# Performance work log

Measured on AMD Instinct MI355X. Metric: run time of the kernel, lower is better.

The kernel has to match this reference:

```python
import jax, jax.numpy as jnp
import numpy as np

N_HEAD = 8
D_MODEL = 512
D_K = 64
D_V = 64


def setup_inputs() -> dict:
    key = jax.random.key(0)
    ks = jax.random.split(key, 12)
    B, L = 2, 2048
    q = jax.random.normal(ks[0], (B, L, D_MODEL), dtype=jnp.float32)
    k = jax.random.normal(ks[1], (B, L, D_MODEL), dtype=jnp.float32)
    v = jax.random.normal(ks[2], (B, L, D_MODEL), dtype=jnp.float32)
    mask = jnp.ones((B, L, L), dtype=jnp.int32)
    s = 1.0 / np.sqrt(D_MODEL)
    Wq = jax.random.uniform(ks[3], (D_MODEL, N_HEAD * D_K), jnp.float32, -s, s)
    bq = jax.random.uniform(ks[4], (N_HEAD * D_K,), jnp.float32, -s, s)
    Wk = jax.random.uniform(ks[5], (D_MODEL, N_HEAD * D_K), jnp.float32, -s, s)
    bk = jax.random.uniform(ks[6], (N_HEAD * D_K,), jnp.float32, -s, s)
    Wv = jax.random.uniform(ks[7], (D_MODEL, N_HEAD * D_V), jnp.float32, -s, s)
    bv = jax.random.uniform(ks[8], (N_HEAD * D_V,), jnp.float32, -s, s)
    so = 1.0 / np.sqrt(N_HEAD * D_V)
    Wo = jax.random.uniform(ks[9], (N_HEAD * D_V, D_MODEL), jnp.float32, -so, so)
    bo = jax.random.uniform(ks[10], (D_MODEL,), jnp.float32, -so, so)
    return {"q": q, "k": k, "v": v, "mask": mask,
            "Wq": Wq, "bq": bq, "Wk": Wk, "bk": bk,
            "Wv": Wv, "bv": bv, "Wo": Wo, "bo": bo}


def reference(q, k, v, mask, Wq, bq, Wk, bk, Wv, bv, Wo, bo):
    B, Lq, _ = q.shape
    Lk = k.shape[1]
    residual = q
    # project and split heads: [B, L, H, d] -> [H, B, L, d]
    qh = (q @ Wq + bq).reshape(B, Lq, N_HEAD, D_K).transpose(2, 0, 1, 3)
    kh = (k @ Wk + bk).reshape(B, Lk, N_HEAD, D_K).transpose(2, 0, 1, 3)
    vh = (v @ Wv + bv).reshape(B, Lk, N_HEAD, D_V).transpose(2, 0, 1, 3)
    # NOTE: original code uses temperature = d_k (not sqrt(d_k))
    attn = jnp.einsum('hbqd,hbkd->hbqk', qh / D_K, kh)
    attn = jnp.where(mask[None, :, :, :] == 0, -1e9, attn)
    attn = jax.nn.softmax(attn, axis=-1)  # dropout is identity at eval
    ctx = jnp.einsum('hbqk,hbkv->hbqv', attn, vh)  # [H, B, Lq, d_v]
    out = ctx.transpose(1, 2, 0, 3).reshape(B, Lq, N_HEAD * D_V)
    out = out @ Wo + bo + residual
    attn_out = attn.reshape(N_HEAD * B, Lq, Lk)  # matches original return layout
    return out, attn_out
```

## Files before the change

kernel.cpp:

```cpp
#include <hip/hip_runtime.h>
#include <hip/hip_bf16.h>
#include <cstdint>
#include <cstddef>

#define NH 8
#define DMODEL 512
#define DHEAD 64
#define BB 2
#define SEQ 2048

typedef __bf16 bf16x8 __attribute__((ext_vector_type(8)));
typedef float f32x4 __attribute__((ext_vector_type(4)));
typedef unsigned short u16;
typedef unsigned int u32;

__device__ __forceinline__ float bf2f(u16 u) {
  return __uint_as_float(((u32)u) << 16);
}
__device__ __forceinline__ u16 f2bf(float f) {
  u32 x = __float_as_uint(f);
  x += 0x7fffu + ((x >> 16) & 1u);
  return (u16)(x >> 16);
}
__device__ __forceinline__ u32 pk2(float lo, float hi) {
  return (u32)f2bf(lo) | ((u32)f2bf(hi) << 16);
}

__global__ __launch_bounds__(256) void transpose_w(
    const float* w0, const float* w1, const float* w2, const float* w3,
    u16* o0, u16* o1, u16* o2, u16* o3) {
  __shared__ u16 t[64][72];
  const float* srcs[4] = {w0, w1, w2, w3};
  u16* dsts[4] = {o0, o1, o2, o3};
  int z = blockIdx.z;
  int r0 = blockIdx.y * 64, c0 = blockIdx.x * 64;
  const float* src = srcs[z] + (size_t)r0 * DMODEL + c0;
  u16* dst = dsts[z] + (size_t)c0 * DMODEL + r0;
  int tid = threadIdx.x;
#pragma unroll
  for (int p = 0; p < 4; ++p) {
    int c = tid + p * 256;
    int row = c >> 4, cc = (c & 15) * 4;
    float4 f = *(const float4*)(src + (size_t)row * DMODEL + cc);
    t[row][cc + 0] = f2bf(f.x); t[row][cc + 1] = f2bf(f.y);
    t[row][cc + 2] = f2bf(f.z); t[row][cc + 3] = f2bf(f.w);
  }
  __syncthreads();
#pragma unroll
  for (int p = 0; p < 2; ++p) {
    int c = tid + p * 256;
    int n = c >> 3, kc = (c & 7) * 8;
    uint4 w;
    w.x = (u32)t[kc + 0][n] | ((u32)t[kc + 1][n] << 16);
    w.y = (u32)t[kc + 2][n] | ((u32)t[kc + 3][n] << 16);
    w.z = (u32)t[kc + 4][n] | ((u32)t[kc + 5][n] << 16);
    w.w = (u32)t[kc + 6][n] | ((u32)t[kc + 7][n] << 16);
    *(uint4*)(dst + (size_t)n * DMODEL + kc) = w;
  }
}

__global__ __launch_bounds__(256) void transpose_v(const u16* Vp, u16* Vt) {
  __shared__ u16 t[64][72];
  int hb2 = blockIdx.y;
  int b = hb2 >> 3, h = hb2 & 7;
  int kp0 = blockIdx.x * 64;
  const u16* src = Vp + ((size_t)(b * SEQ + kp0)) * DMODEL + h * DHEAD;
  u16* dst = Vt + ((size_t)hb2 * DHEAD) * SEQ + kp0;
  int tid = threadIdx.x;
#pragma unroll
  for (int p = 0; p < 2; ++p) {
    int c = tid + p * 256;
    int row = c >> 3, cc = (c & 7) * 8;
    uint4 w = *(const uint4*)(src + (size_t)row * DMODEL + cc);
    t[row][cc + 0] = (u16)(w.x);  t[row][cc + 1] = (u16)(w.x >> 16);
    t[row][cc + 2] = (u16)(w.y);  t[row][cc + 3] = (u16)(w.y >> 16);
    t[row][cc + 4] = (u16)(w.z);  t[row][cc + 5] = (u16)(w.z >> 16);
    t[row][cc + 6] = (u16)(w.w);  t[row][cc + 7] = (u16)(w.w >> 16);
  }
  __syncthreads();
#pragma unroll
  for (int p = 0; p < 2; ++p) {
    int c = tid + p * 256;
    int n = c >> 3, kc = (c & 7) * 8;
    uint4 w;
    w.x = (u32)t[kc + 0][n] | ((u32)t[kc + 1][n] << 16);
    w.y = (u32)t[kc + 2][n] | ((u32)t[kc + 3][n] << 16);
    w.z = (u32)t[kc + 4][n] | ((u32)t[kc + 5][n] << 16);
    w.w = (u32)t[kc + 6][n] | ((u32)t[kc + 7][n] << 16);
    *(uint4*)(dst + (size_t)n * SEQ + kc) = w;
  }
}

__global__ __launch_bounds__(256) void mask_compress(const int* __restrict__ m,
                                                     u32* __restrict__ bits) {
  size_t e = (size_t)blockIdx.x * 256 + threadIdx.x;
  int lane = threadIdx.x & 63;
  unsigned long long bal = __ballot(m[e] != 0);
  if (lane == 0) bits[e >> 5] = (u32)bal;
  else if (lane == 32) bits[e >> 5] = (u32)(bal >> 32);
}

template <bool AF32, bool YF32>
__device__ __forceinline__ void gemm_body(const void* Xv,
                                          const u16* __restrict__ Wt,
                                          const float* __restrict__ bias,
                                          const float* __restrict__ resid,
                                          void* Yv) {
  __shared__ __align__(16) u16 aL[4 * 128 * 8];
  __shared__ __align__(16) u16 bL[4 * 128 * 8];
  int tid = threadIdx.x;
  int m0 = blockIdx.x * 128, n0 = blockIdx.y * 128;
  int wave = tid >> 6, lane = tid & 63;
  int lane16 = lane & 15, quad = lane >> 4;
  int wrow = (wave >> 1) * 64, wcol = (wave & 1) * 64;
  f32x4 acc[4][4] = {};
  for (int kt = 0; kt < 16; ++kt) {
    int k0 = kt * 32;
#pragma unroll
    for (int p = 0; p < 2; ++p) {
      int c = tid + p * 256;
      int row = c >> 2, kq = c & 3;
      if (AF32) {
        const float* s = (const float*)Xv + (size_t)(m0 + row) * DMODEL + k0 + kq * 8;
        float4 f0 = *(const float4*)(s);
        float4 f1 = *(const float4*)(s + 4);
        uint4 w = make_uint4(pk2(f0.x, f0.y), pk2(f0.z, f0.w),
                             pk2(f1.x, f1.y), pk2(f1.z, f1.w));
        *(uint4*)(aL + (((kq * 128 + row) ^ kq) * 8)) = w;
      } else {
        *(uint4*)(aL + (((kq * 128 + row) ^ kq) * 8)) =
            *(const uint4*)((const u16*)Xv + (size_t)(m0 + row) * DMODEL + k0 + kq * 8);
      }
      *(uint4*)(bL + (((kq * 128 + row) ^ kq) * 8)) =
          *(const uint4*)(Wt + (size_t)(n0 + row) * DMODEL + k0 + kq * 8);
    }
    __syncthreads();
    bf16x8 aF[4], bF[4];
#pragma unroll
    for (int t = 0; t < 4; ++t) {
      aF[t] = *(const bf16x8*)(aL + (((quad * 128 + wrow + t * 16 + lane16) ^ quad) * 8));
      bF[t] = *(const bf16x8*)(bL + (((quad * 128 + wcol + t * 16 + lane16) ^ quad) * 8));
    }
#pragma unroll
    for (int tm = 0; tm < 4; ++tm)
#pragma unroll
      for (int tn = 0; tn < 4; ++tn)
        acc[tm][tn] = __builtin_amdgcn_mfma_f32_16x16x32_bf16(
            aF[tm], bF[tn], acc[tm][tn], 0, 0, 0);
    __syncthreads();
  }
#pragma unroll
  for (int tm = 0; tm < 4; ++tm) {
#pragma unroll
    for (int r = 0; r < 4; ++r) {
      int mm = m0 + wrow + tm * 16 + quad * 4 + r;
#pragma unroll
      for (int tn = 0; tn < 4; ++tn) {
        int n = n0 + wcol + tn * 16 + lane16;
        float v = acc[tm][tn][r] + bias[n];
        if (YF32) {
          ((float*)Yv)[(size_t)mm * DMODEL + n] = v + resid[(size_t)mm * DMODEL + n];
        } else {
          ((u16*)Yv)[(size_t)mm * DMODEL + n] = f2bf(v);
        }
      }
    }
  }
}

__global__ __launch_bounds__(256) void qkv_gemm(
    const float* xq, const float* xk, const float* xv,
    const u16* wtq, const u16* wtk, const u16* wtv,
    const float* bq, const float* bk, const float* bv,
    u16* yq, u16* yk, u16* yv) {
  int z = blockIdx.z;
  const float* X = (z == 0) ? xq : (z == 1) ? xk : xv;
  const u16* Wt = (z == 0) ? wtq : (z == 1) ? wtk : wtv;
  const float* bias = (z == 0) ? bq : (z == 1) ? bk : bv;
  u16* Y = (z == 0) ? yq : (z == 1) ? yk : yv;
  gemm_body<true, false>(X, Wt, bias, nullptr, Y);
}

__global__ __launch_bounds__(256) void out_gemm(const u16* X, const u16* Wt,
                                                const float* bias,
                                                const float* resid, float* Y) {
  gemm_body<false, true>(X, Wt, bias, resid, Y);
}

__global__ __launch_bounds__(256) void attn_flash(
    const u16* __restrict__ Qp, const u16* __restrict__ Kp,
    const u16* __restrict__ Vt, const u32* __restrict__ mbits,
    float* __restrict__ stats, u16* __restrict__ Ctx) {
  __shared__ __align__(16) u16 kL[8 * 128 * 8];
  __shared__ __align__(16) u16 vL[16 * 64 * 8];
  int tid = threadIdx.x;
  int hb = blockIdx.y;
  int h = hb >> 1, b = hb & 1;
  int q0 = blockIdx.x * 64;
  int wave = tid >> 6, lane = tid & 63;
  int lane16 = lane & 15, quad = lane >> 4;
  int qw = wave * 16;

  const u16* Qbase = Qp + ((size_t)(b * SEQ + q0)) * DMODEL + h * DHEAD;
  const u16* Kbase = Kp + ((size_t)b * SEQ) * DMODEL + h * DHEAD;
  const u16* Vbase = Vt + ((size_t)(b * 8 + h) * DHEAD) * SEQ;
  const u32* Mb = mbits + ((size_t)(b * SEQ + q0)) * (SEQ / 32);

#pragma unroll
  for (int p = 0; p < 2; ++p) {
    int c = tid + p * 256;
    int row = c >> 3, kq = c & 7;
    *(uint4*)(kL + (((kq * 64 + row) ^ kq) * 8)) =
        *(const uint4*)(Qbase + (size_t)row * DMODEL + kq * 8);
  }
  __syncthreads();
  int mq = qw + lane16;
  bf16x8 a0 = *(const bf16x8*)(kL + (((quad * 64 + mq) ^ quad) * 8));
  bf16x8 a1 = *(const bf16x8*)(kL + ((((4 + quad) * 64 + mq) ^ (4 + quad)) * 8));

  float mrow[4], lrow[4];
#pragma unroll
  for (int r = 0; r < 4; ++r) { mrow[r] = -1e30f; lrow[r] = 0.f; }
  f32x4 oacc[4] = {};
  const float scale = 1.0f / 64.0f;

  for (int j = 0; j < 16; ++j) {
    int kp0 = j * 128;
    __syncthreads();
#pragma unroll
    for (int p = 0; p < 4; ++p) {
      int c = tid + p * 256;
      int row = c >> 3, dq = c & 7;
      *(uint4*)(kL + (((dq * 128 + row) ^ dq) * 8)) =
          *(const uint4*)(Kbase + (size_t)(kp0 + row) * DMODEL + dq * 8);
      int d = c >> 4, kpq = c & 15;
      *(uint4*)(vL + (((kpq * 64 + d) ^ (kpq & 7)) * 8)) =
          *(const uint4*)(Vbase + (size_t)d * SEQ + kp0 + kpq * 8);
    }
    __syncthreads();
    f32x4 s[8] = {};
    __builtin_amdgcn_s_setprio(1);
#pragma unroll
    for (int tn = 0; tn < 8; ++tn) {
      int rowk = tn * 16 + lane16;
      bf16x8 b0 = *(const bf16x8*)(kL + (((quad * 128 + rowk) ^ quad) * 8));
      bf16x8 b1 = *(const bf16x8*)(kL + ((((4 + quad) * 128 + rowk) ^ (4 + quad)) * 8));
      s[tn] = __builtin_amdgcn_mfma_f32_16x16x32_bf16(a0, b0, s[tn], 0, 0, 0);
      s[tn] = __builtin_amdgcn_mfma_f32_16x16x32_bf16(a1, b1, s[tn], 0, 0, 0);
    }
    __builtin_amdgcn_s_setprio(0);
    float pv[4][8], cf[4];
#pragma unroll
    for (int r = 0; r < 4; ++r) {
      int m = qw + quad * 4 + r;
      uint4 mw = *(const uint4*)(Mb + (size_t)m * (SEQ / 32) + (kp0 >> 5));
      u32 mwv[4] = {mw.x, mw.y, mw.z, mw.w};
      float vmax = -1e30f, sv[8];
#pragma unroll
      for (int tn = 0; tn < 8; ++tn) {
        float x = s[tn][r] * scale;
        if (((mwv[tn >> 1] >> (((tn & 1) << 4) + lane16)) & 1u) == 0u) x = -1e9f;
        sv[tn] = x;
        vmax = fmaxf(vmax, x);
      }
#pragma unroll
      for (int o = 1; o < 16; o <<= 1) vmax = fmaxf(vmax, __shfl_xor(vmax, o));
      float nm = fmaxf(mrow[r], vmax);
      cf[r] = __expf(mrow[r] - nm);
      float se = 0.f;
#pragma unroll
      for (int tn = 0; tn < 8; ++tn) {
        float e = __expf(sv[tn] - nm);
        pv[r][tn] = e;
        se += e;
      }
#pragma unroll
      for (int o = 1; o < 16; o <<= 1) se += __shfl_xor(se, o);
      lrow[r] = lrow[r] * cf[r] + se;
      mrow[r] = nm;
    }
#pragma unroll
    for (int tn = 0; tn < 4; ++tn)
#pragma unroll
      for (int r = 0; r < 4; ++r) oacc[tn][r] *= cf[r];
    __syncthreads();
#pragma unroll
    for (int r = 0; r < 4; ++r) {
      int m = qw + quad * 4 + r;
      int sw = (m >> 2) & 7;
#pragma unroll
      for (int tn = 0; tn < 8; ++tn) {
        int kpl = tn * 16 + lane16;
        kL[((((kpl >> 3) * 64 + m) ^ sw) * 8) + (kpl & 7)] = f2bf(pv[r][tn]);
      }
    }
    __syncthreads();
    __builtin_amdgcn_s_setprio(1);
#pragma unroll
    for (int ks = 0; ks < 4; ++ks) {
      int kpq = ks * 4 + quad;
      bf16x8 aF = *(const bf16x8*)(kL + (((kpq * 64 + mq) ^ ((mq >> 2) & 7)) * 8));
#pragma unroll
      for (int tn = 0; tn < 4; ++tn) {
        bf16x8 bF = *(const bf16x8*)(vL + (((kpq * 64 + tn * 16 + lane16) ^ (kpq & 7)) * 8));
        oacc[tn] = __builtin_amdgcn_mfma_f32_16x16x32_bf16(aF, bF, oacc[tn], 0, 0, 0);
      }
    }
    __builtin_amdgcn_s_setprio(0);
  }
  float rl[4];
#pragma unroll
  for (int r = 0; r < 4; ++r) rl[r] = 1.0f / lrow[r];
#pragma unroll
  for (int tn = 0; tn < 4; ++tn)
#pragma unroll
    for (int r = 0; r < 4; ++r) {
      int qq = q0 + qw + quad * 4 + r;
      int d = tn * 16 + lane16;
      Ctx[((size_t)(b * SEQ + qq)) * DMODEL + h * DHEAD + d] =
          f2bf(oacc[tn][r] * rl[r]);
    }
  if (lane16 == 0) {
#pragma unroll
    for (int r = 0; r < 4; ++r) {
      int qq = q0 + qw + quad * 4 + r;
      ((float2*)stats)[(size_t)hb * SEQ + qq] = make_float2(mrow[r], rl[r]);
    }
  }
}

__global__ __launch_bounds__(256) void attn_probs(
    const u16* __restrict__ Qp, const u16* __restrict__ Kp,
    const u32* __restrict__ mbits, const float* __restrict__ stats,
    float* __restrict__ attnOut) {
  __shared__ __align__(16) u16 qL[8 * 64 * 8];
  __shared__ __align__(16) u16 kL[8 * 128 * 8];
  int tid = threadIdx.x;
  int hb = blockIdx.y;
  int h = hb >> 1, b = hb & 1;
  int q0 = blockIdx.x * 64;
  int kp0 = blockIdx.z * 128;
  int wave = tid >> 6, lane = tid & 63;
  int lane16 = lane & 15, quad = lane >> 4;
  int qw = wave * 16;
  const u16* Qbase = Qp + ((size_t)(b * SEQ + q0)) * DMODEL + h * DHEAD;
  const u16* Kbase = Kp + ((size_t)(b * SEQ + kp0)) * DMODEL + h * DHEAD;
  const u32* Mb = mbits + ((size_t)(b * SEQ + q0)) * (SEQ / 32) + (kp0 >> 5);
#pragma unroll
  for (int p = 0; p < 2; ++p) {
    int c = tid + p * 256;
    int row = c >> 3, kq = c & 7;
    *(uint4*)(qL + (((kq * 64 + row) ^ kq) * 8)) =
        *(const uint4*)(Qbase + (size_t)row * DMODEL + kq * 8);
  }
#pragma unroll
  for (int p = 0; p < 4; ++p) {
    int c = tid + p * 256;
    int row = c >> 3, dq = c & 7;
    *(uint4*)(kL + (((dq * 128 + row) ^ dq) * 8)) =
        *(const uint4*)(Kbase + (size_t)row * DMODEL + dq * 8);
  }
  __syncthreads();
  int mq = qw + lane16;
  bf16x8 a0 = *(const bf16x8*)(qL + (((quad * 64 + mq) ^ quad) * 8));
  bf16x8 a1 = *(const bf16x8*)(qL + ((((4 + quad) * 64 + mq) ^ (4 + quad)) * 8));
  f32x4 s[8] = {};
#pragma unroll
  for (int tn = 0; tn < 8; ++tn) {
    int rowk = tn * 16 + lane16;
    bf16x8 b0 = *(const bf16x8*)(kL + (((quad * 128 + rowk) ^ quad) * 8));
    bf16x8 b1 = *(const bf16x8*)(kL + ((((4 + quad) * 128 + rowk) ^ (4 + quad)) * 8));
    s[tn] = __builtin_amdgcn_mfma_f32_16x16x32_bf16(a0, b0, s[tn], 0, 0, 0);
    s[tn] = __builtin_amdgcn_mfma_f32_16x16x32_bf16(a1, b1, s[tn], 0, 0, 0);
  }
  const float scale = 1.0f / 64.0f;
#pragma unroll
  for (int r = 0; r < 4; ++r) {
    int m = qw + quad * 4 + r;
    float2 st = ((const float2*)stats)[(size_t)hb * SEQ + q0 + m];
    uint4 mw = *(const uint4*)(Mb + (size_t)m * (SEQ / 32));
    u32 mwv[4] = {mw.x, mw.y, mw.z, mw.w};
    float* dst = attnOut + ((size_t)hb * SEQ + q0 + m) * SEQ + kp0 + lane16;
#pragma unroll
    for (int tn = 0; tn < 8; ++tn) {
      float x = s[tn][r] * scale;
      if (((mwv[tn >> 1] >> (((tn & 1) << 4) + lane16)) & 1u) == 0u) x = -1e9f;
      __builtin_nontemporal_store(__expf(x - st.x) * st.y, dst + tn * 16);
    }
  }
}

extern "C" void kernel_launch(void* const* d_in, const int* in_sizes, int n_in,
                              void* d_out, int out_size, void* d_ws,
                              size_t ws_size, hipStream_t stream) {
  const float* q = (const float*)d_in[0];
  const float* k = (const float*)d_in[1];
  const float* v = (const float*)d_in[2];
  const int* mask = (const int*)d_in[3];
  const float* Wq = (const float*)d_in[4];
  const float* bq = (const float*)d_in[5];
  const float* Wk = (const float*)d_in[6];
  const float* bk = (const float*)d_in[7];
  const float* Wv = (const float*)d_in[8];
  const float* bv = (const float*)d_in[9];
  const float* Wo = (const float*)d_in[10];
  const float* bo = (const float*)d_in[11];

  u16* ws = (u16*)d_ws;
  u16* wtq = ws + 0;
  u16* wtk = ws + 262144;
  u16* wtv = ws + 524288;
  u16* wto = ws + 786432;
  u16* Qp  = ws + 1048576;
  u16* Kp  = ws + 3145728;
  u16* Vp  = ws + 5242880;
  u16* Vt  = ws + 7340032;
  u16* Ctx = ws + 9437184;
  float* stats = (float*)(ws + 5242880);
  u32* mbits   = (u32*)(ws + 5242880 + 131072);

  float* outp = (float*)d_out;
  float* attnp = outp + (size_t)BB * SEQ * DMODEL;

  transpose_w<<<dim3(8, 8, 4), 256, 0, stream>>>(Wq, Wk, Wv, Wo,
                                                 wtq, wtk, wtv, wto);
  qkv_gemm<<<dim3(32, 4, 3), 256, 0, stream>>>(q, k, v, wtq, wtk, wtv,
                                               bq, bk, bv, Qp, Kp, Vp);
  transpose_v<<<dim3(32, 16), 256, 0, stream>>>(Vp, Vt);
  mask_compress<<<dim3((BB * SEQ * SEQ) / 256), 256, 0, stream>>>(mask, mbits);
  attn_flash<<<dim3(32, 16), 256, 0, stream>>>(Qp, Kp, Vt, mbits, stats, Ctx);
  attn_probs<<<dim3(32, 16, 16), 256, 0, stream>>>(Qp, Kp, mbits, stats, attnp);
  out_gemm<<<dim3(32, 4), 256, 0, stream>>>(Ctx, wto, bo, q, outp);
}
```

Before: 498.1 us.

## Fuse prep kernels and software-pipeline GEMM and flash attention tile loads

Merges the weight transpose, a new fp32-to-bf16 activation conversion, and the mask bit-compression into a single prep launch. The mask compressor now packs 32 ints per thread with vector loads instead of a wavefront ballot. The GEMM gets double-buffered LDS with register prefetch of the next K tile. The flash kernel prefetches the next K/V tile into registers during compute and hoists mask and stats loads. The aim is to cut launch count and hide global load latency, at the cost of an extra bf16 activation buffer, more workspace and higher register pressure.

```diff
diff --git a/kernel.cpp b/kernel.cpp
--- a/kernel.cpp
+++ b/kernel.cpp
@@ -26,36 +26,64 @@
   return (u32)f2bf(lo) | ((u32)f2bf(hi) << 16);
 }
 
-__global__ __launch_bounds__(256) void transpose_w(
-    const float* w0, const float* w1, const float* w2, const float* w3,
-    u16* o0, u16* o1, u16* o2, u16* o3) {
+__global__ __launch_bounds__(256) void prep(
+    const float* Wq, const float* Wk, const float* Wv, const float* Wo,
+    u16* wtq, u16* wtk, u16* wtv, u16* wto,
+    const float* xq, const float* xk, const float* xv,
+    u16* Xq, u16* Xk, u16* Xv,
+    const int* __restrict__ mask, u32* __restrict__ mbits) {
   __shared__ u16 t[64][72];
-  const float* srcs[4] = {w0, w1, w2, w3};
-  u16* dsts[4] = {o0, o1, o2, o3};
-  int z = blockIdx.z;
-  int r0 = blockIdx.y * 64, c0 = blockIdx.x * 64;
-  const float* src = srcs[z] + (size_t)r0 * DMODEL + c0;
-  u16* dst = dsts[z] + (size_t)c0 * DMODEL + r0;
-  int tid = threadIdx.x;
-#pragma unroll
-  for (int p = 0; p < 4; ++p) {
-    int c = tid + p * 256;
-    int row = c >> 4, cc = (c & 15) * 4;
-    float4 f = *(const float4*)(src + (size_t)row * DMODEL + cc);
-    t[row][cc + 0] = f2bf(f.x); t[row][cc + 1] = f2bf(f.y);
-    t[row][cc + 2] = f2bf(f.z); t[row][cc + 3] = f2bf(f.w);
-  }
-  __syncthreads();
-#pragma unroll
-  for (int p = 0; p < 2; ++p) {
-    int c = tid + p * 256;
-    int n = c >> 3, kc = (c & 7) * 8;
-    uint4 w;
-    w.x = (u32)t[kc + 0][n] | ((u32)t[kc + 1][n] << 16);
-    w.y = (u32)t[kc + 2][n] | ((u32)t[kc + 3][n] << 16);
-    w.z = (u32)t[kc + 4][n] | ((u32)t[kc + 5][n] << 16);
-    w.w = (u32)t[kc + 6][n] | ((u32)t[kc + 7][n] << 16);
-    *(uint4*)(dst + (size_t)n * DMODEL + kc) = w;
+  int bid = blockIdx.x, tid = threadIdx.x;
+  if (bid < 256) {
+    const float* srcs[4] = {Wq, Wk, Wv, Wo};
+    u16* dsts[4] = {wtq, wtk, wtv, wto};
+    int z = bid >> 6, tile = bid & 63;
+    int r0 = (tile >> 3) * 64, c0 = (tile & 7) * 64;
+    const float* src = srcs[z] + (size_t)r0 * DMODEL + c0;
+    u16* dst = dsts[z] + (size_t)c0 * DMODEL + r0;
+#pragma unroll
+    for (int p = 0; p < 4; ++p) {
+      int c = tid + p * 256;
+      int row = c >> 4, cc = (c & 15) * 4;
+      float4 f = *(const float4*)(src + (size_t)row * DMODEL + cc);
+      t[row][cc + 0] = f2bf(f.x); t[row][cc + 1] = f2bf(f.y);
+      t[row][cc + 2] = f2bf(f.z); t[row][cc + 3] = f2bf(f.w);
+    }
+    __syncthreads();
+#pragma unroll
+    for (int p = 0; p < 2; ++p) {
+      int c = tid + p * 256;
+      int n = c >> 3, kc = (c & 7) * 8;
+      uint4 w;
+      w.x = (u32)t[kc + 0][n] | ((u32)t[kc + 1][n] << 16);
+      w.y = (u32)t[kc + 2][n] | ((u32)t[kc + 3][n] << 16);
+      w.z = (u32)t[kc + 4][n] | ((u32)t[kc + 5][n] << 16);
+      w.w = (u32)t[kc + 6][n] | ((u32)t[kc + 7][n] << 16);
+      *(uint4*)(dst + (size_t)n * DMODEL + kc) = w;
+    }
+  } else if (bid < 3328) {
+    int id = bid - 256;
+    const float* src = (id < 1024) ? xq : (id < 2048) ? xk : xv;
+    u16* dst = (id < 1024) ? Xq : (id < 2048) ? Xk : Xv;
+    size_t off = (size_t)(id & 1023) * 2048 + (size_t)tid * 8;
+    float4 f0 = *(const float4*)(src + off);
+    float4 f1 = *(const float4*)(src + off + 4);
+    uint4 w = make_uint4(pk2(f0.x, f0.y), pk2(f0.z, f0.w),
+                         pk2(f1.x, f1.y), pk2(f1.z, f1.w));
+    *(uint4*)(dst + off) = w;
+  } else {
+    size_t w0 = (size_t)(bid - 3328) * 256 + tid;
+    const int* mp = mask + w0 * 32;
+    u32 bits = 0;
+#pragma unroll
+    for (int c = 0; c < 8; ++c) {
+      uint4 v = *(const uint4*)(mp + c * 4);
+      bits |= (v.x != 0 ? 1u : 0u) << (c * 4 + 0);
+      bits |= (v.y != 0 ? 1u : 0u) << (c * 4 + 1);
+      bits |= (v.z != 0 ? 1u : 0u) << (c * 4 + 2);
+      bits |= (v.w != 0 ? 1u : 0u) << (c * 4 + 3);
+    }
+    mbits[w0] = bits;
   }
 }
 
@@ -91,55 +119,50 @@
   }
 }
 
-__global__ __launch_bounds__(256) void mask_compress(const int* __restrict__ m,
-                                                     u32* __restrict__ bits) {
-  size_t e = (size_t)blockIdx.x * 256 + threadIdx.x;
-  int lane = threadIdx.x & 63;
-  unsigned long long bal = __ballot(m[e] != 0);
-  if (lane == 0) bits[e >> 5] = (u32)bal;
-  else if (lane == 32) bits[e >> 5] = (u32)(bal >> 32);
-}
-
-template <bool AF32, bool YF32>
-__device__ __forceinline__ void gemm_body(const void* Xv,
+template <bool YF32>
+__device__ __forceinline__ void gemm_body(const u16* __restrict__ X,
                                           const u16* __restrict__ Wt,
                                           const float* __restrict__ bias,
                                           const float* __restrict__ resid,
                                           void* Yv) {
-  __shared__ __align__(16) u16 aL[4 * 128 * 8];
-  __shared__ __align__(16) u16 bL[4 * 128 * 8];
+  __shared__ __align__(16) u16 aL[2][4 * 128 * 8];
+  __shared__ __align__(16) u16 bL[2][4 * 128 * 8];
   int tid = threadIdx.x;
   int m0 = blockIdx.x * 128, n0 = blockIdx.y * 128;
   int wave = tid >> 6, lane = tid & 63;
   int lane16 = lane & 15, quad = lane >> 4;
   int wrow = (wave >> 1) * 64, wcol = (wave & 1) * 64;
+  int row0 = tid >> 2, kq0 = tid & 3;
+  const u16* Abase = X + (size_t)m0 * DMODEL;
+  const u16* Bbase = Wt + (size_t)n0 * DMODEL;
+  uint4 ra0, ra1, rb0, rb1;
+  auto issue = [&](int kt) {
+    int k0 = kt * 32;
+    const u16* ap = Abase + (size_t)row0 * DMODEL + k0 + kq0 * 8;
+    const u16* bp = Bbase + (size_t)row0 * DMODEL + k0 + kq0 * 8;
+    ra0 = *(const uint4*)(ap);
+    rb0 = *(const uint4*)(bp);
+    ra1 = *(const uint4*)(ap + (size_t)64 * DMODEL);
+    rb1 = *(const uint4*)(bp + (size_t)64 * DMODEL);
+  };
+  auto commit = [&](int b) {
+    *(uint4*)(aL[b] + (((kq0 * 128 + row0) ^ kq0) * 8)) = ra0;
+    *(uint4*)(bL[b] + (((kq0 * 128 + row0) ^ kq0) * 8)) = rb0;
+    *(uint4*)(aL[b] + (((kq0 * 128 + row0 + 64) ^ kq0) * 8)) = ra1;
+    *(uint4*)(bL[b] + (((kq0 * 128 + row0 + 64) ^ kq0) * 8)) = rb1;
+  };
   f32x4 acc[4][4] = {};
+  issue(0);
+  commit(0);
+  __syncthreads();
   for (int kt = 0; kt < 16; ++kt) {
-    int k0 = kt * 32;
-#pragma unroll
-    for (int p = 0; p < 2; ++p) {
-      int c = tid + p * 256;
-      int row = c >> 2, kq = c & 3;
-      if (AF32) {
-        const float* s = (const float*)Xv + (size_t)(m0 + row) * DMODEL + k0 + kq * 8;
-        float4 f0 = *(const float4*)(s);
-        float4 f1 = *(const float4*)(s + 4);
-        uint4 w = make_uint4(pk2(f0.x, f0.y), pk2(f0.z, f0.w),
-                             pk2(f1.x, f1.y), pk2(f1.z, f1.w));
-        *(uint4*)(aL + (((kq * 128 + row) ^ kq) * 8)) = w;
-      } else {
-        *(uint4*)(aL + (((kq * 128 + row) ^ kq) * 8)) =
-            *(const uint4*)((const u16*)Xv + (size_t)(m0 + row) * DMODEL + k0 + kq * 8);
-      }
-      *(uint4*)(bL + (((kq * 128 + row) ^ kq) * 8)) =
-          *(const uint4*)(Wt + (size_t)(n0 + row) * DMODEL + k0 + kq * 8);
-    }
-    __syncthreads();
+    if (kt < 15) issue(kt + 1);
+    int b = kt & 1;
     bf16x8 aF[4], bF[4];
 #pragma unroll
     for (int t = 0; t < 4; ++t) {
-      aF[t] = *(const bf16x8*)(aL + (((quad * 128 + wrow + t * 16 + lane16) ^ quad) * 8));
-      bF[t] = *(const bf16x8*)(bL + (((quad * 128 + wcol + t * 16 + lane16) ^ quad) * 8));
+      aF[t] = *(const bf16x8*)(aL[b] + (((quad * 128 + wrow + t * 16 + lane16) ^ quad) * 8));
+      bF[t] = *(const bf16x8*)(bL[b] + (((quad * 128 + wcol + t * 16 + lane16) ^ quad) * 8));
     }
 #pragma unroll
     for (int tm = 0; tm < 4; ++tm)
@@ -147,6 +170,7 @@
       for (int tn = 0; tn < 4; ++tn)
         acc[tm][tn] = __builtin_amdgcn_mfma_f32_16x16x32_bf16(
             aF[tm], bF[tn], acc[tm][tn], 0, 0, 0);
+    if (kt < 15) commit((kt + 1) & 1);
     __syncthreads();
   }
 #pragma unroll
@@ -169,22 +193,22 @@
 }
 
 __global__ __launch_bounds__(256) void qkv_gemm(
-    const float* xq, const float* xk, const float* xv,
+    const u16* Xq, const u16* Xk, const u16* Xv,
     const u16* wtq, const u16* wtk, const u16* wtv,
     const float* bq, const float* bk, const float* bv,
     u16* yq, u16* yk, u16* yv) {
   int z = blockIdx.z;
-  const float* X = (z == 0) ? xq : (z == 1) ? xk : xv;
+  const u16* X = (z == 0) ? Xq : (z == 1) ? Xk : Xv;
   const u16* Wt = (z == 0) ? wtq : (z == 1) ? wtk : wtv;
   const float* bias = (z == 0) ? bq : (z == 1) ? bk : bv;
   u16* Y = (z == 0) ? yq : (z == 1) ? yk : yv;
-  gemm_body<true, false>(X, Wt, bias, nullptr, Y);
+  gemm_body<false>(X, Wt, bias, nullptr, Y);
 }
 
 __global__ __launch_bounds__(256) void out_gemm(const u16* X, const u16* Wt,
                                                 const float* bias,
                                                 const float* resid, float* Y) {
-  gemm_body<false, true>(X, Wt, bias, resid, Y);
+  gemm_body<true>(X, Wt, bias, resid, Y);
 }
 
 __global__ __launch_bounds__(256) void attn_flash(
@@ -206,6 +230,29 @@
   const u16* Vbase = Vt + ((size_t)(b * 8 + h) * DHEAD) * SEQ;
   const u32* Mb = mbits + ((size_t)(b * SEQ + q0)) * (SEQ / 32);
 
+  uint4 rk[4], rv[4];
+  auto issueKV = [&](int j) {
+    int kp0 = j * 128;
+#pragma unroll
+    for (int p = 0; p < 4; ++p) {
+      int c = tid + p * 256;
+      int row = c >> 3, dq = c & 7;
+      rk[p] = *(const uint4*)(Kbase + (size_t)(kp0 + row) * DMODEL + dq * 8);
+      int d = c >> 4, kpq = c & 15;
+      rv[p] = *(const uint4*)(Vbase + (size_t)d * SEQ + kp0 + kpq * 8);
+    }
+  };
+  auto commitKV = [&]() {
+#pragma unroll
+    for (int p = 0; p < 4; ++p) {
+      int c = tid + p * 256;
+      int row = c >> 3, dq = c & 7;
+      *(uint4*)(kL + (((dq * 128 + row) ^ dq) * 8)) = rk[p];
+      int d = c >> 4, kpq = c & 15;
+      *(uint4*)(vL + (((kpq * 64 + d) ^ (kpq & 7)) * 8)) = rv[p];
+    }
+  };
+
 #pragma unroll
   for (int p = 0; p < 2; ++p) {
     int c = tid + p * 256;
@@ -217,6 +264,10 @@
   int mq = qw + lane16;
   bf16x8 a0 = *(const bf16x8*)(kL + (((quad * 64 + mq) ^ quad) * 8));
   bf16x8 a1 = *(const bf16x8*)(kL + ((((4 + quad) * 64 + mq) ^ (4 + quad)) * 8));
+  issueKV(0);
+  __syncthreads();
+  commitKV();
+  __syncthreads();
 
   float mrow[4], lrow[4];
 #pragma unroll
@@ -226,18 +277,11 @@
 
   for (int j = 0; j < 16; ++j) {
     int kp0 = j * 128;
-    __syncthreads();
-#pragma unroll
-    for (int p = 0; p < 4; ++p) {
-      int c = tid + p * 256;
-      int row = c >> 3, dq = c & 7;
-      *(uint4*)(kL + (((dq * 128 + row) ^ dq) * 8)) =
-          *(const uint4*)(Kbase + (size_t)(kp0 + row) * DMODEL + dq * 8);
-      int d = c >> 4, kpq = c & 15;
-      *(uint4*)(vL + (((kpq * 64 + d) ^ (kpq & 7)) * 8)) =
-          *(const uint4*)(Vbase + (size_t)d * SEQ + kp0 + kpq * 8);
-    }
-    __syncthreads();
+    if (j < 15) issueKV(j + 1);
+    uint4 mw[4];
+#pragma unroll
+    for (int r = 0; r < 4; ++r)
+      mw[r] = *(const uint4*)(Mb + (size_t)(qw + quad * 4 + r) * (SEQ / 32) + (kp0 >> 5));
     f32x4 s[8] = {};
     __builtin_amdgcn_s_setprio(1);
 #pragma unroll
@@ -252,9 +296,7 @@
     float pv[4][8], cf[4];
 #pragma unroll
     for (int r = 0; r < 4; ++r) {
-      int m = qw + quad * 4 + r;
-      uint4 mw = *(const uint4*)(Mb + (size_t)m * (SEQ / 32) + (kp0 >> 5));
-      u32 mwv[4] = {mw.x, mw.y, mw.z, mw.w};
+      u32 mwv[4] = {mw[r].x, mw[r].y, mw[r].z, mw[r].w};
       float vmax = -1e30f, sv[8];
 #pragma unroll
       for (int tn = 0; tn < 8; ++tn) {
@@ -307,6 +349,11 @@
       }
     }
     __builtin_amdgcn_s_setprio(0);
+    __syncthreads();
+    if (j < 15) {
+      commitKV();
+      __syncthreads();
+    }
   }
   float rl[4];
 #pragma unroll
@@ -360,6 +407,14 @@
     *(uint4*)(kL + (((dq * 128 + row) ^ dq) * 8)) =
         *(const uint4*)(Kbase + (size_t)row * DMODEL + dq * 8);
   }
+  float2 st[4];
+  uint4 mw[4];
+#pragma unroll
+  for (int r = 0; r < 4; ++r) {
+    int m = qw + quad * 4 + r;
+    st[r] = ((const float2*)stats)[(size_t)hb * SEQ + q0 + m];
+    mw[r] = *(const uint4*)(Mb + (size_t)m * (SEQ / 32));
+  }
   __syncthreads();
   int mq = qw + lane16;
   bf16x8 a0 = *(const bf16x8*)(qL + (((quad * 64 + mq) ^ quad) * 8));
@@ -377,15 +432,13 @@
 #pragma unroll
   for (int r = 0; r < 4; ++r) {
     int m = qw + quad * 4 + r;
-    float2 st = ((const float2*)stats)[(size_t)hb * SEQ + q0 + m];
-    uint4 mw = *(const uint4*)(Mb + (size_t)m * (SEQ / 32));
-    u32 mwv[4] = {mw.x, mw.y, mw.z, mw.w};
+    u32 mwv[4] = {mw[r].x, mw[r].y, mw[r].z, mw[r].w};
     float* dst = attnOut + ((size_t)hb * SEQ + q0 + m) * SEQ + kp0 + lane16;
 #pragma unroll
     for (int tn = 0; tn < 8; ++tn) {
       float x = s[tn][r] * scale;
       if (((mwv[tn >> 1] >> (((tn & 1) << 4) + lane16)) & 1u) == 0u) x = -1e9f;
-      __builtin_nontemporal_store(__expf(x - st.x) * st.y, dst + tn * 16);
+      __builtin_nontemporal_store(__expf(x - st[r].x) * st[r].y, dst + tn * 16);
     }
   }
 }
@@ -411,23 +464,25 @@
   u16* wtk = ws + 262144;
   u16* wtv = ws + 524288;
   u16* wto = ws + 786432;
-  u16* Qp  = ws + 1048576;
-  u16* Kp  = ws + 3145728;
-  u16* Vp  = ws + 5242880;
-  u16* Vt  = ws + 7340032;
-  u16* Ctx = ws + 9437184;
-  float* stats = (float*)(ws + 5242880);
-  u32* mbits   = (u32*)(ws + 5242880 + 131072);
+  u16* Xq  = ws + 1048576;
+  u16* Xk  = ws + 3145728;
+  u16* Xv  = ws + 5242880;
+  u16* Qp  = ws + 7340032;
+  u16* Kp  = ws + 9437184;
+  u16* Vp  = ws + 11534336;
+  u16* Vt  = ws + 13631488;
+  u16* Ctx = ws + 15728640;
+  float* stats = (float*)(ws + 17825792);
+  u32* mbits   = (u32*)(ws + 17956864);
 
   float* outp = (float*)d_out;
   float* attnp = outp + (size_t)BB * SEQ * DMODEL;
 
-  transpose_w<<<dim3(8, 8, 4), 256, 0, stream>>>(Wq, Wk, Wv, Wo,
-                                                 wtq, wtk, wtv, wto);
-  qkv_gemm<<<dim3(32, 4, 3), 256, 0, stream>>>(q, k, v, wtq, wtk, wtv,
+  prep<<<dim3(4352), 256, 0, stream>>>(Wq, Wk, Wv, Wo, wtq, wtk, wtv, wto,
+                                       q, k, v, Xq, Xk, Xv, mask, mbits);
+  qkv_gemm<<<dim3(32, 4, 3), 256, 0, stream>>>(Xq, Xk, Xv, wtq, wtk, wtv,
                                                bq, bk, bv, Qp, Kp, Vp);
   transpose_v<<<dim3(32, 16), 256, 0, stream>>>(Vp, Vt);
-  mask_compress<<<dim3((BB * SEQ * SEQ) / 256), 256, 0, stream>>>(mask, mbits);
   attn_flash<<<dim3(32, 16), 256, 0, stream>>>(Qp, Kp, Vt, mbits, stats, Ctx);
   attn_probs<<<dim3(32, 16, 16), 256, 0, stream>>>(Qp, Kp, mbits, stats, attnp);
   out_gemm<<<dim3(32, 4), 256, 0, stream>>>(Ctx, wto, bo, q, outp);
```

Result: slower. 536.3 us (+7.7%).
